# Performance work log

Hardware: AMD Instinct MI355X
Metric: run time of the kernel (lower is better)

## Reference

```python
import jax, jax.numpy as jnp
import numpy as np
from jax.ops import segment_sum

N = 50000        # nodes
E = 800000       # edges (avg degree 16)
H = 128          # hidden_dim
N_ITER = 2       # BCRefinement n_iterations
TIE_P = 0.05     # fraction of tie (boundary) edges


def setup_inputs() -> dict:
    key = jax.random.key(0)
    ks = jax.random.split(key, 24)
    s = 0.02
    inp = {
        'h': jax.random.normal(ks[0], (N, H), jnp.float32),
        'e': jax.random.normal(ks[1], (E, H), jnp.float32),
        'edge_attr_raw': jax.random.normal(ks[2], (E, 10), jnp.float32),
        # edge_refine: Linear(3H,2H) -> ReLU -> Linear(2H,H)
        'W_er1': s * jax.random.normal(ks[3], (3 * H, 2 * H), jnp.float32),
        'b_er1': jnp.zeros((2 * H,), jnp.float32),
        'W_er2': s * jax.random.normal(ks[4], (2 * H, H), jnp.float32),
        'b_er2': jnp.zeros((H,), jnp.float32),
        # GRUCell(H,H) torch layout: [3H, H] chunks (r, z, n)
        'W_ih': s * jax.random.normal(ks[5], (3 * H, H), jnp.float32),
        'W_hh': s * jax.random.normal(ks[6], (3 * H, H), jnp.float32),
        'b_ih': jnp.zeros((3 * H,), jnp.float32),
        'b_hh': jnp.zeros((3 * H,), jnp.float32),
        # node_neigh_fc: Linear(H,H)
        'W_nn': s * jax.random.normal(ks[7], (H, H), jnp.float32),
        'b_nn': jnp.zeros((H,), jnp.float32),
        # gate_mlp: Linear(3H,H) -> ReLU -> Linear(H,1), last bias init -2.0
        'W_g1': s * jax.random.normal(ks[8], (3 * H, H), jnp.float32),
        'b_g1': jnp.zeros((H,), jnp.float32),
        'W_g2': s * jax.random.normal(ks[9], (H, 1), jnp.float32),
        'b_g2': jnp.full((1,), -2.0, jnp.float32),
        'edge_index': jax.random.randint(ks[10], (2, E), 0, N, jnp.int32),
        'is_tie': jax.random.uniform(ks[11], (E,)) < TIE_P,
    }
    return inp


def reference(h, e, edge_attr_raw,
              W_er1, b_er1, W_er2, b_er2,
              W_ih, W_hh, b_ih, b_hh,
              W_nn, b_nn,
              W_g1, b_g1, W_g2, b_g2,
              edge_index, is_tie):
    row = edge_index[0]
    col = edge_index[1]
    tie_f = is_tie.astype(h.dtype)                        # [E]
    internal = ~is_tie

    # coupling buses: endpoints of any tie edge (tie-incidence count > 0)
    cpl_cnt = segment_sum(tie_f, row, num_segments=N) + \
              segment_sum(tie_f, col, num_segments=N)     # [N]
    is_cpl = cpl_cnt > 0

    # internal edges pointing into coupling buses; b_smooth weights w = 1/sqrt(X^2+eps)
    to_cpl = internal & is_cpl[col]
    X = jnp.abs(edge_attr_raw[:, 1])
    w = jnp.where(to_cpl, 1.0 / jnp.sqrt(X * X + 1e-6), 0.0)
    w_den = segment_sum(w, col, num_segments=N)           # [N]
    w_norm = w / (w_den[col] + 1e-6)                      # [E], zero off-mask

    deg = jnp.maximum(cpl_cnt, 1.0)                       # clamp_min(1.0)

    h_work, e_work = h, e
    for _ in range(N_ITER):
        # --- tie-edge refinement (applied only on tie edges) ---
        edge_in = jnp.concatenate([e_work, h_work[row], h_work[col]], axis=-1)  # [E,3H]
        e_ref = jax.nn.relu(edge_in @ W_er1 + b_er1) @ W_er2 + b_er2            # [E,H]
        e_work = e_work + tie_f[:, None] * e_ref

        # --- node messages from internal neighbors into coupling buses ---
        m_node_msg = h_work[row] @ W_nn + b_nn                                   # [E,H]
        m_node_all = segment_sum(m_node_msg * w_norm[:, None], col,
                                 num_segments=N)                                 # [N,H]

        # --- mean of incident tie-edge features at each node ---
        tie_e = tie_f[:, None] * e_work                                          # [E,H]
        m_edge_all = (segment_sum(tie_e, row, num_segments=N) +
                      segment_sum(tie_e, col, num_segments=N)) / deg[:, None]    # [N,H]

        # --- gating + GRU update on coupling buses ---
        gate_in = jnp.concatenate([m_edge_all, m_node_all, h_work], axis=-1)     # [N,3H]
        gate = jax.nn.sigmoid(jax.nn.relu(gate_in @ W_g1 + b_g1) @ W_g2 + b_g2)  # [N,1]
        m = m_edge_all + gate * m_node_all                                       # [N,H]

        gi = m @ W_ih.T + b_ih                                                   # [N,3H]
        gh = h_work @ W_hh.T + b_hh
        r = jax.nn.sigmoid(gi[:, :H] + gh[:, :H])
        z = jax.nn.sigmoid(gi[:, H:2 * H] + gh[:, H:2 * H])
        n = jnp.tanh(gi[:, 2 * H:] + r * gh[:, 2 * H:])
        h_new = (1.0 - z) * n + z * h_work

        h_work = jnp.where(is_cpl[:, None], h_new, h_work)
    return h_work, e_work
```

## Files before the change

kernel.cpp:

```cpp
#include <hip/hip_runtime.h>
#include <cstdint>

#define N_NODES 50000
#define N_EDGES 800000
#define HDIM    128
#define TIE_CAP 44000
#define NITER   2
#define SCAN_B  256

typedef __attribute__((ext_vector_type(8))) short bf16x8;
typedef __attribute__((ext_vector_type(4))) float f32x4;

__device__ __forceinline__ uint32_t f2bf(float f) {
    uint32_t u = __builtin_bit_cast(uint32_t, f);
    return (u + 0x7fffu + ((u >> 16) & 1u)) >> 16;
}
__device__ __forceinline__ float bf2f(uint32_t b) {
    return __builtin_bit_cast(float, b << 16);
}
__device__ __forceinline__ uint32_t comb2(uint32_t me, uint32_t mn, float g) {
    float a0 = bf2f(me & 0xffffu) + g * bf2f(mn & 0xffffu);
    float a1 = bf2f(me >> 16)     + g * bf2f(mn >> 16);
    return f2bf(a0) | (f2bf(a1) << 16);
}


__device__ __forceinline__ void stage_a128(const float* __restrict__ base,
                                           const int* __restrict__ gidx,
                                           int m0, int Mlim, char* tile, int tid)
{
    const int c = tid & 15;
    #pragma unroll
    for (int p = 0; p < 4; ++p) {
        int row = p * 32 + (tid >> 4);
        int ar = m0 + row; if (ar >= Mlim) ar = Mlim - 1;
        long g = gidx ? gidx[ar] : ar;
        const float* s = base + g * HDIM + c * 4;
        float4 v0 = *(const float4*)s;
        float4 v1 = *(const float4*)(s + 64);
        uint2 w0 = make_uint2(f2bf(v0.x) | (f2bf(v0.y) << 16),
                              f2bf(v0.z) | (f2bf(v0.w) << 16));
        uint2 w1 = make_uint2(f2bf(v1.x) | (f2bf(v1.y) << 16),
                              f2bf(v1.z) | (f2bf(v1.w) << 16));
        int sw = (row & 7) << 4;
        *(uint2*)(tile + row * 256 + ((c * 8) ^ sw)) = w0;
        *(uint2*)(tile + row * 256 + ((c * 8 + 128) ^ sw)) = w1;
    }
}

__device__ __forceinline__ void stage_bf128(const uint16_t* __restrict__ base,
                                            const int* __restrict__ gidx,
                                            int m0, int Mlim, char* tile, int tid)
{
    const int c = tid & 15;
    #pragma unroll
    for (int p = 0; p < 4; ++p) {
        int row = p * 32 + (tid >> 4);
        int ar = m0 + row; if (ar >= Mlim) ar = Mlim - 1;
        long g = gidx ? gidx[ar] : ar;
        uint4 v = *(const uint4*)(base + g * HDIM + c * 8);
        *(uint4*)(tile + row * 256 + ((c * 16) ^ ((row & 7) << 4))) = v;
    }
}

__device__ __forceinline__ void stage_b128(const short* __restrict__ BT, int ldk,
                                           int n0, int k0, char* tile, int tid)
{
    const int c = tid & 15;
    #pragma unroll
    for (int p = 0; p < 4; ++p) {
        int n = p * 32 + (tid >> 4);
        uint4 v = *(const uint4*)&BT[(size_t)(n0 + n) * ldk + k0 + c * 8];
        *(uint4*)(tile + n * 256 + ((c * 16) ^ ((n & 7) << 4))) = v;
    }
}

__device__ __forceinline__ void mfma128(const char* At, const char* Bt,
                                        int wr, int wc, int lane, f32x4 acc[4][2])
{
    #pragma unroll
    for (int ks = 0; ks < 4; ++ks) {
        int kb = ks * 64 + (lane >> 4) * 16;
        bf16x8 aF[4], bF[2];
        #pragma unroll
        for (int mi = 0; mi < 4; ++mi) {
            int row = wr * 64 + mi * 16 + (lane & 15);
            aF[mi] = *(const bf16x8*)(At + row * 256 + (kb ^ ((row & 7) << 4)));
        }
        #pragma unroll
        for (int ni = 0; ni < 2; ++ni) {
            int n = wc * 32 + ni * 16 + (lane & 15);
            bF[ni] = *(const bf16x8*)(Bt + n * 256 + (kb ^ ((n & 7) << 4)));
        }
        #pragma unroll
        for (int mi = 0; mi < 4; ++mi)
            #pragma unroll
            for (int ni = 0; ni < 2; ++ni)
                acc[mi][ni] = __builtin_amdgcn_mfma_f32_16x16x32_bf16(
                    aF[mi], bF[ni], acc[mi][ni], 0, 0, 0);
    }
}

__global__ __launch_bounds__(512)
void k_tie_fused(float* __restrict__ out_e, const uint16_t* __restrict__ h_bf,
                 const int* __restrict__ tie_cnt_p,
                 const int* __restrict__ tie_list, const int* __restrict__ tie_row,
                 const int* __restrict__ tie_col,
                 const short* __restrict__ BTer1, const short* __restrict__ BTer2,
                 const float* __restrict__ b_er1, const float* __restrict__ b_er2,
                 const float* __restrict__ deg_inv, float* __restrict__ m_edge)
{
    int cnt = *tie_cnt_p; if (cnt > TIE_CAP) cnt = TIE_CAP;
    const int m0 = blockIdx.x * 128;
    if (m0 >= cnt) return;

    __shared__ __align__(16) char At[32 * 1024];
    __shared__ __align__(16) char B0[32 * 1024];
    __shared__ __align__(16) char B1[32 * 1024];

    const int tid = threadIdx.x, lane = tid & 63;
    const int wid = tid >> 6, wr = wid >> 2, wc = wid & 3;

    f32x4 acc0[4][2] = {}, acc1[4][2] = {};
    #pragma unroll 1
    for (int c = 0; c < 3; ++c) {
        if (c == 0) stage_a128(out_e, tie_list, m0, cnt, At, tid);
        else        stage_bf128(h_bf, (c == 1) ? tie_row : tie_col, m0, cnt, At, tid);
        stage_b128(BTer1, 384, 0,   c * 128, B0, tid);
        stage_b128(BTer1, 384, 128, c * 128, B1, tid);
        __syncthreads();
        mfma128(At, B0, wr, wc, lane, acc0);
        mfma128(At, B1, wr, wc, lane, acc1);
        __syncthreads();
    }

    #pragma unroll
    for (int half = 0; half < 2; ++half) {
        char* Ct = half ? B0 : At;
        #pragma unroll
        for (int ni = 0; ni < 2; ++ni) {
            int col = wc * 32 + ni * 16 + (lane & 15);
            float bv = b_er1[half * 128 + col];
            #pragma unroll
            for (int mi = 0; mi < 4; ++mi)
                #pragma unroll
                for (int j = 0; j < 4; ++j) {
                    int rl = wr * 64 + mi * 16 + ((lane >> 4) << 2) + j;
                    float v = fmaxf((half ? acc1 : acc0)[mi][ni][j] + bv, 0.f);
                    *(uint16_t*)(Ct + rl * 256 + ((col * 2) ^ ((rl & 7) << 4))) =
                        (uint16_t)f2bf(v);
                }
        }
    }
    stage_b128(BTer2, 256, 0, 0, B1, tid);
    __syncthreads();
    f32x4 acc2[4][2] = {};
    mfma128(At, B1, wr, wc, lane, acc2);
    __syncthreads();
    stage_b128(BTer2, 256, 0, 128, B1, tid);
    __syncthreads();
    mfma128(B0, B1, wr, wc, lane, acc2);

    int col0 = wc * 32 + (lane & 15);
    float bv0 = b_er2[col0], bv1 = b_er2[col0 + 16];
    #pragma unroll
    for (int mi = 0; mi < 4; ++mi) {
        #pragma unroll
        for (int j = 0; j < 4; ++j) {
            int i = m0 + wr * 64 + mi * 16 + ((lane >> 4) << 2) + j;
            if (i < cnt) {
                int e = tie_list[i], r = tie_row[i], cc = tie_col[i];
                float dr = deg_inv[r], dc = deg_inv[cc];
                #pragma unroll
                for (int ni = 0; ni < 2; ++ni) {
                    int col = col0 + ni * 16;
                    float er = acc2[mi][ni][j] + (ni ? bv1 : bv0);
                    size_t eb = (size_t)e * HDIM + col;
                    float v = out_e[eb] + er;
                    out_e[eb] = v;
                    atomicAdd(&m_edge[(size_t)r * HDIM + col], v * dr);
                    atomicAdd(&m_edge[(size_t)cc * HDIM + col], v * dc);
                }
            }
        }
    }
}

__global__ __launch_bounds__(512)
void k_node_mega(float* __restrict__ m_edge, const uint16_t* __restrict__ agg,
                 float* __restrict__ out_h, uint16_t* __restrict__ h_bf,
                 const float* __restrict__ cpl_cnt, const float* __restrict__ sumw,
                 const short* __restrict__ BTnn, const float* __restrict__ b_nn,
                 const short* __restrict__ BTg1, const float* __restrict__ b_g1,
                 const float* __restrict__ Wg2, const float* __restrict__ b_g2,
                 const short* __restrict__ BTcomb,
                 const short* __restrict__ BTihn, const short* __restrict__ BThhn,
                 const float* __restrict__ b_ih, const float* __restrict__ b_hh)
{
    const int m0 = blockIdx.x * 128;
    __shared__ __align__(16) char Tme[32 * 1024];
    __shared__ __align__(16) char Tmn[32 * 1024];
    __shared__ __align__(16) char Th [32 * 1024];
    __shared__ __align__(16) char Bt [32 * 1024];
    __shared__ float g_red[4][128];
    __shared__ float g_fin[128];
    __shared__ float sw_s[128];

    const int tid = threadIdx.x, lane = tid & 63;
    const int wid = tid >> 6, wr = wid >> 2, wc = wid & 3;

    stage_a128(m_edge, nullptr, m0, N_NODES, Tme, tid);
    stage_bf128(agg,   nullptr, m0, N_NODES, Tmn, tid);
    stage_bf128(h_bf,  nullptr, m0, N_NODES, Th,  tid);
    stage_b128(BTnn, 128, 0, 0, Bt, tid);
    if (tid < 128) {
        int n = m0 + tid; if (n >= N_NODES) n = N_NODES - 1;
        sw_s[tid] = sumw[n];
    }
    __syncthreads();

    {
        int lim = (N_NODES - m0 < 128 ? N_NODES - m0 : 128) * HDIM / 4;
        float4* mp = (float4*)(m_edge + (size_t)m0 * HDIM);
        for (int i2 = tid; i2 < lim; i2 += 512)
            mp[i2] = make_float4(0.f, 0.f, 0.f, 0.f);
    }

    {
        f32x4 accM[4][2] = {};
        mfma128(Tmn, Bt, wr, wc, lane, accM);
        __syncthreads();
        #pragma unroll
        for (int ni = 0; ni < 2; ++ni) {
            int col = wc * 32 + ni * 16 + (lane & 15);
            float bv = b_nn[col];
            #pragma unroll
            for (int mi = 0; mi < 4; ++mi)
                #pragma unroll
                for (int j = 0; j < 4; ++j) {
                    int rl = wr * 64 + mi * 16 + ((lane >> 4) << 2) + j;
                    float v = accM[mi][ni][j] + sw_s[rl] * bv;
                    *(uint16_t*)(Tmn + rl * 256 + ((col * 2) ^ ((rl & 7) << 4))) =
                        (uint16_t)f2bf(v);
                }
        }
        __syncthreads();
    }

    f32x4 accG[4][2] = {};
    #pragma unroll 1
    for (int c = 0; c < 3; ++c) {
        const char* Ac = (c == 0) ? Tme : (c == 1) ? Tmn : Th;
        stage_b128(BTg1, 384, 0, c * 128, Bt, tid);
        __syncthreads();
        mfma128(Ac, Bt, wr, wc, lane, accG);
        __syncthreads();
    }
    {
        float bg[2], wg[2];
        #pragma unroll
        for (int ni = 0; ni < 2; ++ni) {
            int col = wc * 32 + ni * 16 + (lane & 15);
            bg[ni] = b_g1[col]; wg[ni] = Wg2[col];
        }
        #pragma unroll
        for (int mi = 0; mi < 4; ++mi)
            #pragma unroll
            for (int j = 0; j < 4; ++j) {
                float p = fmaxf(accG[mi][0][j] + bg[0], 0.f) * wg[0]
                        + fmaxf(accG[mi][1][j] + bg[1], 0.f) * wg[1];
                #pragma unroll
                for (int o = 8; o; o >>= 1) p += __shfl_xor(p, o);
                if ((lane & 15) == 0)
                    g_red[wc][wr * 64 + mi * 16 + ((lane >> 4) << 2) + j] = p;
            }
    }
    __syncthreads();
    if (tid < 128) {
        float t = g_red[0][tid] + g_red[1][tid] + g_red[2][tid] + g_red[3][tid]
                + b_g2[0];
        g_fin[tid] = 1.f / (1.f + __expf(-t));
    }
    __syncthreads();

    {
        const int c = tid & 15;
        #pragma unroll
        for (int p = 0; p < 4; ++p) {
            int row = p * 32 + (tid >> 4);
            float g = g_fin[row];
            int sw = (row & 7) << 4;
            #pragma unroll
            for (int hh = 0; hh < 2; ++hh) {
                int off = (c * 8 + hh * 128) ^ sw;
                uint2 me2 = *(uint2*)(Tme + row * 256 + off);
                uint2 mn2 = *(uint2*)(Tmn + row * 256 + off);
                *(uint2*)(Tmn + row * 256 + off) =
                    make_uint2(comb2(me2.x, mn2.x, g), comb2(me2.y, mn2.y, g));
            }
        }
    }
    __syncthreads();

    f32x4 aR[4][2] = {}, aZ[4][2] = {}, aGI[4][2] = {}, aGH[4][2] = {};
    stage_b128(BTcomb, 256, 0, 0, Bt, tid);   __syncthreads();
    mfma128(Tmn, Bt, wr, wc, lane, aR);       __syncthreads();
    stage_b128(BTcomb, 256, 0, 128, Bt, tid); __syncthreads();
    mfma128(Th, Bt, wr, wc, lane, aR);        __syncthreads();
    stage_b128(BTcomb, 256, 128, 0, Bt, tid); __syncthreads();
    mfma128(Tmn, Bt, wr, wc, lane, aZ);       __syncthreads();
    stage_b128(BTcomb, 256, 128, 128, Bt, tid); __syncthreads();
    mfma128(Th, Bt, wr, wc, lane, aZ);        __syncthreads();
    stage_b128(BTihn, 128, 0, 0, Bt, tid);    __syncthreads();
    mfma128(Tmn, Bt, wr, wc, lane, aGI);      __syncthreads();
    stage_b128(BThhn, 128, 0, 0, Bt, tid);    __syncthreads();
    mfma128(Th, Bt, wr, wc, lane, aGH);

    #pragma unroll
    for (int ni = 0; ni < 2; ++ni) {
        int col = wc * 32 + ni * 16 + (lane & 15);
        float br  = b_ih[col] + b_hh[col];
        float bz  = b_ih[128 + col] + b_hh[128 + col];
        float bin = b_ih[256 + col], bhn = b_hh[256 + col];
        #pragma unroll
        for (int mi = 0; mi < 4; ++mi)
            #pragma unroll
            for (int j = 0; j < 4; ++j) {
                int node = m0 + wr * 64 + mi * 16 + ((lane >> 4) << 2) + j;
                if (node < N_NODES && cpl_cnt[node] > 0.f) {
                    float r = 1.f / (1.f + __expf(-(aR[mi][ni][j] + br)));
                    float z = 1.f / (1.f + __expf(-(aZ[mi][ni][j] + bz)));
                    float nn = tanhf(aGI[mi][ni][j] + bin + r * (aGH[mi][ni][j] + bhn));
                    size_t hb = (size_t)node * HDIM + col;
                    float hv = out_h[hb];
                    float hn = (1.f - z) * nn + z * hv;
                    out_h[hb] = hn;
                    h_bf[hb] = (uint16_t)f2bf(hn);
                }
            }
    }
}

__global__ __launch_bounds__(256)
void k_mnode_gather(const int* __restrict__ row_ptr, const int* __restrict__ csr_row,
                    const float* __restrict__ csr_w, const uint16_t* __restrict__ h_bf,
                    uint16_t* __restrict__ agg)
{
    int n = blockIdx.x * 4 + (threadIdx.x >> 6);
    if (n >= N_NODES) return;
    int lane = threadIdx.x & 63;
    int s = row_ptr[n], t = row_ptr[n + 1];
    float a0 = 0.f, a1 = 0.f;
    for (int j = s; j < t; ++j) {
        int r = csr_row[j];
        float w = csr_w[j];
        uint32_t v = *(const uint32_t*)(h_bf + (size_t)r * HDIM + lane * 2);
        a0 += w * bf2f(v & 0xffffu);
        a1 += w * bf2f(v >> 16);
    }
    *(uint32_t*)(agg + (size_t)n * HDIM + lane * 2) = f2bf(a0) | (f2bf(a1) << 16);
}

#define INIT_BLOCKS 2753

__global__ __launch_bounds__(256)
void k_init(const float* __restrict__ e, float* __restrict__ out_e,
            const float* __restrict__ h, float* __restrict__ out_h,
            uint16_t* __restrict__ h_bf, float* __restrict__ m_edge,
            float* __restrict__ cpl_cnt, float* __restrict__ w_den,
            int* __restrict__ hist, int* __restrict__ counters,
            const uint8_t* __restrict__ tie_raw,
            const float* __restrict__ W_er1, const float* __restrict__ W_er2,
            const float* __restrict__ W_nn, const float* __restrict__ W_g1,
            const float* __restrict__ W_ih, const float* __restrict__ W_hh,
            short* __restrict__ BTer1, short* __restrict__ BTer2,
            short* __restrict__ BTnn, short* __restrict__ BTg1,
            short* __restrict__ BTcomb, short* __restrict__ BTihn,
            short* __restrict__ BThhn)
{
    const int b = blockIdx.x, t = threadIdx.x;
    if (b < 2048) {
        const float4* src = (const float4*)e;
        float4* dst = (float4*)out_e;
        for (int i = b * 256 + t; i < N_EDGES * HDIM / 4; i += 2048 * 256)
            dst[i] = src[i];
    } else if (b < 2304) {
        for (int i = (b - 2048) * 256 + t; i < N_NODES * HDIM / 4; i += 256 * 256) {
            float4 v = ((const float4*)h)[i];
            ((float4*)out_h)[i] = v;
            *(uint2*)(h_bf + (size_t)i * 4) =
                make_uint2(f2bf(v.x) | (f2bf(v.y) << 16),
                           f2bf(v.z) | (f2bf(v.w) << 16));
        }
    } else if (b < 2560) {
        for (int i = (b - 2304) * 256 + t; i < N_NODES * HDIM / 4; i += 256 * 256)
            ((float4*)m_edge)[i] = make_float4(0.f, 0.f, 0.f, 0.f);
    } else if (b < 2624) {
        for (int i = (b - 2560) * 256 + t; i < N_NODES; i += 64 * 256) {
            cpl_cnt[i] = 0.f; w_den[i] = 0.f; hist[i] = 0;
        }
    } else if (b < 2752) {
        for (int i = (b - 2624) * 256 + t; i < 384 * 256; i += 128 * 256) {
            {   int n = i / 384, k = i % 384;
                BTer1[i] = (short)f2bf(W_er1[(size_t)k * 256 + n]); }
            if (i < 128 * 256) {
                int n = i / 256, k = i % 256;
                BTer2[i] = (short)f2bf(W_er2[(size_t)k * 128 + n]); }
            if (i < 128 * 128) {
                int n = i / 128, k = i % 128;
                BTnn[i] = (short)f2bf(W_nn[(size_t)k * 128 + n]); }
            if (i < 128 * 384) {
                int n = i / 384, k = i % 384;
                BTg1[i] = (short)f2bf(W_g1[(size_t)k * 128 + n]); }
            if (i < 256 * 256) {
                int n = i >> 8, k = i & 255;
                float v = (k < 128) ? W_ih[n * 128 + k] : W_hh[n * 128 + (k - 128)];
                BTcomb[i] = (short)f2bf(v); }
            if (i < 128 * 128) {
                BTihn[i] = (short)f2bf(W_ih[256 * 128 + i]);
                BThhn[i] = (short)f2bf(W_hh[256 * 128 + i]); }
        }
    } else {
        if (t < 64) {
            int c = 0;
            for (int k = t; k < 4096; k += 64)
                if ((k & 3) && tie_raw[k]) c = 1;
            unsigned long long m = __ballot(c != 0);
            if (t == 0) {
                counters[0] = (m != 0ull) ? 1 : 0;
                counters[1] = 0; counters[2] = 0;
            }
        }
    }
}

__global__ __launch_bounds__(256)
void k_tie(const void* __restrict__ tie_raw, const int* __restrict__ counters,
           const int* __restrict__ ei, float* __restrict__ cpl_cnt,
           int* __restrict__ tie_cnt, int* __restrict__ tie_list,
           int* __restrict__ tie_row, int* __restrict__ tie_col)
{
    int e = blockIdx.x * 256 + threadIdx.x;
    int fmt = counters[0];
    bool t = false; int r = 0, c = 0;
    if (e < N_EDGES)
        t = fmt ? (((const uint8_t*)tie_raw)[e] != 0)
                : (((const int*)tie_raw)[e] != 0);
    if (t) {
        r = ei[e]; c = ei[N_EDGES + e];
        atomicAdd(&cpl_cnt[r], 1.f);
        atomicAdd(&cpl_cnt[c], 1.f);
    }
    unsigned long long m = __ballot(t);
    if (m == 0ull) return;
    int lane = threadIdx.x & 63;
    int first = __ffsll((unsigned long long)m) - 1;
    int base = 0;
    if (lane == first) base = atomicAdd(tie_cnt, __popcll(m));
    base = __shfl(base, first);
    if (t) {
        int idx = base + __popcll(m & ((1ull << lane) - 1ull));
        if (idx < TIE_CAP) { tie_list[idx] = e; tie_row[idx] = r; tie_col[idx] = c; }
    }
}

__global__ __launch_bounds__(256)
void k_w(const void* __restrict__ tie_raw, const int* __restrict__ counters,
         const int* __restrict__ ei, const float* __restrict__ attr,
         const float* __restrict__ cpl_cnt, float* __restrict__ w_den,
         float* __restrict__ w_arr, int* __restrict__ hist)
{
    int e = blockIdx.x * 256 + threadIdx.x;
    if (e >= N_EDGES) return;
    int fmt = counters[0];
    bool t = fmt ? (((const uint8_t*)tie_raw)[e] != 0)
                 : (((const int*)tie_raw)[e] != 0);
    float w = 0.f;
    if (!t) {
        int c = ei[N_EDGES + e];
        if (cpl_cnt[c] > 0.f) {
            float X = fabsf(attr[(size_t)e * 10 + 1]);
            w = 1.f / sqrtf(X * X + 1e-6f);
            atomicAdd(&w_den[c], w);
            atomicAdd(&hist[c], 1);
        }
    }
    w_arr[e] = w;
}

__global__ __launch_bounds__(SCAN_B)
void k_scan1(const int* __restrict__ hist, int* __restrict__ excl,
             int* __restrict__ bsum)
{
    __shared__ int s[SCAN_B];
    int t = threadIdx.x;
    int i = blockIdx.x * SCAN_B + t;
    int v = (i < N_NODES) ? hist[i] : 0;
    s[t] = v;
    __syncthreads();
    for (int o = 1; o < SCAN_B; o <<= 1) {
        int u = (t >= o) ? s[t - o] : 0;
        __syncthreads();
        s[t] += u;
        __syncthreads();
    }
    if (i < N_NODES) excl[i] = s[t] - v;
    if (t == SCAN_B - 1) bsum[blockIdx.x] = s[t];
}

__global__ void k_scan2(int* __restrict__ bsum, int* __restrict__ counters)
{
    const int NB = (N_NODES + SCAN_B - 1) / SCAN_B;
    if (threadIdx.x == 0) {
        int run = 0;
        for (int b = 0; b < NB; ++b) { int x = bsum[b]; bsum[b] = run; run += x; }
        counters[2] = run;
    }
}

__global__ __launch_bounds__(256)
void k_scan3(const int* __restrict__ excl, const int* __restrict__ bsum,
             int* __restrict__ row_ptr, int* __restrict__ cursor,
             const int* __restrict__ counters,
             const float* __restrict__ cpl_cnt, const float* __restrict__ w_den,
             float* __restrict__ deg_inv, float* __restrict__ sumw)
{
    int i = blockIdx.x * 256 + threadIdx.x;
    if (i < N_NODES) {
        int v = excl[i] + bsum[i >> 8];
        row_ptr[i] = v;
        cursor[i] = v;
        deg_inv[i] = 1.f / fmaxf(cpl_cnt[i], 1.f);
        float wd = w_den[i];
        sumw[i] = wd / (wd + 1e-6f);
    }
    if (i == N_NODES) row_ptr[N_NODES] = counters[2];
}

__global__ __launch_bounds__(256)
void k_fill(const int* __restrict__ ei, const float* __restrict__ w_arr,
            const float* __restrict__ w_den, int* __restrict__ cursor,
            int* __restrict__ csr_row, float* __restrict__ csr_w)
{
    int e = blockIdx.x * 256 + threadIdx.x;
    if (e >= N_EDGES) return;
    float w = w_arr[e];
    if (w == 0.f) return;
    int c = ei[N_EDGES + e];
    int pos = atomicAdd(&cursor[c], 1);
    csr_row[pos] = ei[e];
    csr_w[pos] = w / (w_den[c] + 1e-6f);
}

extern "C" void kernel_launch(void* const* d_in, const int* in_sizes, int n_in,
                              void* d_out, int out_size, void* d_ws, size_t ws_size,
                              hipStream_t stream)
{
    const float* h     = (const float*)d_in[0];
    const float* e     = (const float*)d_in[1];
    const float* attr  = (const float*)d_in[2];
    const float* W_er1 = (const float*)d_in[3];
    const float* b_er1 = (const float*)d_in[4];
    const float* W_er2 = (const float*)d_in[5];
    const float* b_er2 = (const float*)d_in[6];
    const float* W_ih  = (const float*)d_in[7];
    const float* W_hh  = (const float*)d_in[8];
    const float* b_ih  = (const float*)d_in[9];
    const float* b_hh  = (const float*)d_in[10];
    const float* W_nn  = (const float*)d_in[11];
    const float* b_nn  = (const float*)d_in[12];
    const float* W_g1  = (const float*)d_in[13];
    const float* b_g1  = (const float*)d_in[14];
    const float* W_g2  = (const float*)d_in[15];
    const float* b_g2  = (const float*)d_in[16];
    const int*   ei    = (const int*)d_in[17];
    const void*  tie_raw = d_in[18];

    float* out_h = (float*)d_out;
    float* out_e = out_h + (size_t)N_NODES * HDIM;

    char* ws = (char*)d_ws;
    size_t off = 0;
    auto alloc = [&](size_t bytes) -> void* {
        void* p = ws + off;
        off = (off + bytes + 255) & ~(size_t)255;
        return p;
    };
    float* cpl_cnt = (float*)alloc((size_t)N_NODES * 4);
    float* w_den   = (float*)alloc((size_t)N_NODES * 4);
    int*   hist    = (int*)  alloc((size_t)N_NODES * 4);
    int*   counters= (int*)  alloc(256);
    float* deg_inv = (float*)alloc((size_t)N_NODES * 4);
    float* sumw    = (float*)alloc((size_t)N_NODES * 4);
    float* w_arr   = (float*)alloc((size_t)N_EDGES * 4);
    int* tie_list  = (int*)alloc((size_t)TIE_CAP * 4);
    int* tie_row   = (int*)alloc((size_t)TIE_CAP * 4);
    int* tie_col   = (int*)alloc((size_t)TIE_CAP * 4);
    short* BTer1   = (short*)alloc((size_t)256 * 384 * 2);
    short* BTer2   = (short*)alloc((size_t)128 * 256 * 2);
    short* BTnn    = (short*)alloc((size_t)128 * 128 * 2);
    short* BTg1    = (short*)alloc((size_t)128 * 384 * 2);
    short* BTcomb  = (short*)alloc((size_t)256 * 256 * 2);
    short* BTihn   = (short*)alloc((size_t)128 * 128 * 2);
    short* BThhn   = (short*)alloc((size_t)128 * 128 * 2);
    uint16_t* h_bf = (uint16_t*)alloc((size_t)N_NODES * HDIM * 2);
    uint16_t* agg  = (uint16_t*)alloc((size_t)N_NODES * HDIM * 2);
    float* m_edge  = (float*)alloc((size_t)N_NODES * HDIM * 4);
    int* excl      = (int*)alloc((size_t)N_NODES * 4);
    int* bsum      = (int*)alloc(256 * 4);
    int* row_ptr   = (int*)alloc((size_t)(N_NODES + 1) * 4);
    int* cursor    = (int*)alloc((size_t)N_NODES * 4);
    int* csr_row   = (int*)alloc((size_t)N_EDGES * 4);
    float* csr_w   = (float*)alloc((size_t)N_EDGES * 4);
    if (off > ws_size) return;

    int* tie_cnt = counters + 1;

    const int EB   = N_EDGES / 256;
    const int GM_T = (TIE_CAP + 127) / 128;
    const int GM_N = (N_NODES + 127) / 128;
    const int NB   = (N_NODES + SCAN_B - 1) / SCAN_B;

    k_init<<<INIT_BLOCKS, 256, 0, stream>>>(
        e, out_e, h, out_h, h_bf, m_edge, cpl_cnt, w_den, hist, counters,
        (const uint8_t*)tie_raw,
        W_er1, W_er2, W_nn, W_g1, W_ih, W_hh,
        BTer1, BTer2, BTnn, BTg1, BTcomb, BTihn, BThhn);
    k_tie<<<EB, 256, 0, stream>>>(tie_raw, counters, ei, cpl_cnt,
                                  tie_cnt, tie_list, tie_row, tie_col);
    k_w<<<EB, 256, 0, stream>>>(tie_raw, counters, ei, attr, cpl_cnt,
                                w_den, w_arr, hist);
    k_scan1<<<NB, SCAN_B, 0, stream>>>(hist, excl, bsum);
    k_scan2<<<1, 64, 0, stream>>>(bsum, counters);
    k_scan3<<<(N_NODES + 256) / 256, 256, 0, stream>>>(
        excl, bsum, row_ptr, cursor, counters, cpl_cnt, w_den, deg_inv, sumw);
    k_fill<<<EB, 256, 0, stream>>>(ei, w_arr, w_den, cursor, csr_row, csr_w);

    for (int it = 0; it < NITER; ++it) {
        k_tie_fused<<<GM_T, 512, 0, stream>>>(
            out_e, h_bf, tie_cnt, tie_list, tie_row, tie_col,
            BTer1, BTer2, b_er1, b_er2, deg_inv, m_edge);
        k_mnode_gather<<<(N_NODES + 3) / 4, 256, 0, stream>>>(
            row_ptr, csr_row, csr_w, h_bf, agg);
        k_node_mega<<<GM_N, 512, 0, stream>>>(
            m_edge, agg, out_h, h_bf, cpl_cnt, sumw,
            BTnn, b_nn, BTg1, b_g1, W_g2, b_g2,
            BTcomb, BTihn, BThhn, b_ih, b_hh);
    }
}
```

Baseline: 911.6 us.

## Replace tie-edge atomic scatter with CSR gather and double-buffer GRU weight staging

Builds a second CSR indexing tie edges by incident node during setup. The per-node mean of tie-edge features is now gathered inside the m_node gather kernel instead of being scatter-added with float atomics in the tie GEMM epilogue. That removes the fp32 m_edge buffer, its zeroing passes and the atomics, and stores the mean in bf16. The node kernel also alternates two shared buffers for weight staging so fewer barriers are needed between MFMA phases. The costs are an extra scan and fill pass and a bf16 rounding of the edge mean.

```diff
diff --git a/kernel.cpp b/kernel.cpp
--- a/kernel.cpp
+++ b/kernel.cpp
@@ -7,6 +7,8 @@
 #define TIE_CAP 44000
 #define NITER   2
 #define SCAN_B  256
+#define EB_CONST 3125
+#define TB_CONST 172
 
 typedef __attribute__((ext_vector_type(8))) short bf16x8;
 typedef __attribute__((ext_vector_type(4))) float f32x4;
@@ -107,8 +109,7 @@
                  const int* __restrict__ tie_list, const int* __restrict__ tie_row,
                  const int* __restrict__ tie_col,
                  const short* __restrict__ BTer1, const short* __restrict__ BTer2,
-                 const float* __restrict__ b_er1, const float* __restrict__ b_er2,
-                 const float* __restrict__ deg_inv, float* __restrict__ m_edge)
+                 const float* __restrict__ b_er1, const float* __restrict__ b_er2)
 {
     int cnt = *tie_cnt_p; if (cnt > TIE_CAP) cnt = TIE_CAP;
     const int m0 = blockIdx.x * 128;
@@ -169,25 +170,56 @@
         for (int j = 0; j < 4; ++j) {
             int i = m0 + wr * 64 + mi * 16 + ((lane >> 4) << 2) + j;
             if (i < cnt) {
-                int e = tie_list[i], r = tie_row[i], cc = tie_col[i];
-                float dr = deg_inv[r], dc = deg_inv[cc];
+                int e = tie_list[i];
                 #pragma unroll
                 for (int ni = 0; ni < 2; ++ni) {
                     int col = col0 + ni * 16;
-                    float er = acc2[mi][ni][j] + (ni ? bv1 : bv0);
                     size_t eb = (size_t)e * HDIM + col;
-                    float v = out_e[eb] + er;
-                    out_e[eb] = v;
-                    atomicAdd(&m_edge[(size_t)r * HDIM + col], v * dr);
-                    atomicAdd(&m_edge[(size_t)cc * HDIM + col], v * dc);
+                    out_e[eb] += acc2[mi][ni][j] + (ni ? bv1 : bv0);
                 }
             }
         }
     }
 }
 
+__global__ __launch_bounds__(256)
+void k_gather(const int* __restrict__ row_ptr, const int* __restrict__ csr_row,
+              const float* __restrict__ csr_w, const uint16_t* __restrict__ h_bf,
+              uint16_t* __restrict__ agg,
+              const int* __restrict__ row_ptr2, const int* __restrict__ tcsr,
+              const float* __restrict__ out_e, const float* __restrict__ deg_inv,
+              uint16_t* __restrict__ m_edge_bf)
+{
+    int n = blockIdx.x * 4 + (threadIdx.x >> 6);
+    if (n >= N_NODES) return;
+    int lane = threadIdx.x & 63;
+
+    int s = row_ptr[n], t = row_ptr[n + 1];
+    float a0 = 0.f, a1 = 0.f;
+    for (int j = s; j < t; ++j) {
+        int r = csr_row[j];
+        float w = csr_w[j];
+        uint32_t v = *(const uint32_t*)(h_bf + (size_t)r * HDIM + lane * 2);
+        a0 += w * bf2f(v & 0xffffu);
+        a1 += w * bf2f(v >> 16);
+    }
+    *(uint32_t*)(agg + (size_t)n * HDIM + lane * 2) = f2bf(a0) | (f2bf(a1) << 16);
+
+    int s2 = row_ptr2[n], t2 = row_ptr2[n + 1];
+    float b0 = 0.f, b1 = 0.f;
+    for (int j = s2; j < t2; ++j) {
+        int e = tcsr[j];
+        float2 v = *(const float2*)(out_e + (size_t)e * HDIM + lane * 2);
+        b0 += v.x; b1 += v.y;
+    }
+    float di = deg_inv[n];
+    *(uint32_t*)(m_edge_bf + (size_t)n * HDIM + lane * 2) =
+        f2bf(b0 * di) | (f2bf(b1 * di) << 16);
+}
+
 __global__ __launch_bounds__(512)
-void k_node_mega(float* __restrict__ m_edge, const uint16_t* __restrict__ agg,
+void k_node_mega(const uint16_t* __restrict__ m_edge_bf,
+                 const uint16_t* __restrict__ agg,
                  float* __restrict__ out_h, uint16_t* __restrict__ h_bf,
                  const float* __restrict__ cpl_cnt, const float* __restrict__ sumw,
                  const short* __restrict__ BTnn, const float* __restrict__ b_nn,
@@ -209,22 +241,15 @@
     const int tid = threadIdx.x, lane = tid & 63;
     const int wid = tid >> 6, wr = wid >> 2, wc = wid & 3;
 
-    stage_a128(m_edge, nullptr, m0, N_NODES, Tme, tid);
-    stage_bf128(agg,   nullptr, m0, N_NODES, Tmn, tid);
-    stage_bf128(h_bf,  nullptr, m0, N_NODES, Th,  tid);
+    stage_bf128(m_edge_bf, nullptr, m0, N_NODES, Tme, tid);
+    stage_bf128(agg,       nullptr, m0, N_NODES, Tmn, tid);
+    stage_bf128(h_bf,      nullptr, m0, N_NODES, Th,  tid);
     stage_b128(BTnn, 128, 0, 0, Bt, tid);
     if (tid < 128) {
         int n = m0 + tid; if (n >= N_NODES) n = N_NODES - 1;
         sw_s[tid] = sumw[n];
     }
     __syncthreads();
-
-    {
-        int lim = (N_NODES - m0 < 128 ? N_NODES - m0 : 128) * HDIM / 4;
-        float4* mp = (float4*)(m_edge + (size_t)m0 * HDIM);
-        for (int i2 = tid; i2 < lim; i2 += 512)
-            mp[i2] = make_float4(0.f, 0.f, 0.f, 0.f);
-    }
 
     {
         f32x4 accM[4][2] = {};
@@ -283,6 +308,7 @@
     }
     __syncthreads();
 
+    stage_b128(BTcomb, 256, 0, 0, Bt, tid);
     {
         const int c = tid & 15;
         #pragma unroll
@@ -303,18 +329,17 @@
     __syncthreads();
 
     f32x4 aR[4][2] = {}, aZ[4][2] = {}, aGI[4][2] = {}, aGH[4][2] = {};
-    stage_b128(BTcomb, 256, 0, 0, Bt, tid);   __syncthreads();
-    mfma128(Tmn, Bt, wr, wc, lane, aR);       __syncthreads();
-    stage_b128(BTcomb, 256, 0, 128, Bt, tid); __syncthreads();
-    mfma128(Th, Bt, wr, wc, lane, aR);        __syncthreads();
-    stage_b128(BTcomb, 256, 128, 0, Bt, tid); __syncthreads();
-    mfma128(Tmn, Bt, wr, wc, lane, aZ);       __syncthreads();
-    stage_b128(BTcomb, 256, 128, 128, Bt, tid); __syncthreads();
-    mfma128(Th, Bt, wr, wc, lane, aZ);        __syncthreads();
-    stage_b128(BTihn, 128, 0, 0, Bt, tid);    __syncthreads();
-    mfma128(Tmn, Bt, wr, wc, lane, aGI);      __syncthreads();
-    stage_b128(BThhn, 128, 0, 0, Bt, tid);    __syncthreads();
-    mfma128(Th, Bt, wr, wc, lane, aGH);
+    stage_b128(BTcomb, 256, 0, 128, Tme, tid);
+    mfma128(Tmn, Bt, wr, wc, lane, aR);   __syncthreads();
+    stage_b128(BTcomb, 256, 128, 0, Bt, tid);
+    mfma128(Th, Tme, wr, wc, lane, aR);   __syncthreads();
+    stage_b128(BTcomb, 256, 128, 128, Tme, tid);
+    mfma128(Tmn, Bt, wr, wc, lane, aZ);   __syncthreads();
+    stage_b128(BTihn, 128, 0, 0, Bt, tid);
+    mfma128(Th, Tme, wr, wc, lane, aZ);   __syncthreads();
+    stage_b128(BThhn, 128, 0, 0, Tme, tid);
+    mfma128(Tmn, Bt, wr, wc, lane, aGI);  __syncthreads();
+    mfma128(Th, Tme, wr, wc, lane, aGH);
 
     #pragma unroll
     for (int ni = 0; ni < 2; ++ni) {
@@ -341,32 +366,12 @@
     }
 }
 
-__global__ __launch_bounds__(256)
-void k_mnode_gather(const int* __restrict__ row_ptr, const int* __restrict__ csr_row,
-                    const float* __restrict__ csr_w, const uint16_t* __restrict__ h_bf,
-                    uint16_t* __restrict__ agg)
-{
-    int n = blockIdx.x * 4 + (threadIdx.x >> 6);
-    if (n >= N_NODES) return;
-    int lane = threadIdx.x & 63;
-    int s = row_ptr[n], t = row_ptr[n + 1];
-    float a0 = 0.f, a1 = 0.f;
-    for (int j = s; j < t; ++j) {
-        int r = csr_row[j];
-        float w = csr_w[j];
-        uint32_t v = *(const uint32_t*)(h_bf + (size_t)r * HDIM + lane * 2);
-        a0 += w * bf2f(v & 0xffffu);
-        a1 += w * bf2f(v >> 16);
-    }
-    *(uint32_t*)(agg + (size_t)n * HDIM + lane * 2) = f2bf(a0) | (f2bf(a1) << 16);
-}
-
-#define INIT_BLOCKS 2753
+#define INIT_BLOCKS 2497
 
 __global__ __launch_bounds__(256)
 void k_init(const float* __restrict__ e, float* __restrict__ out_e,
             const float* __restrict__ h, float* __restrict__ out_h,
-            uint16_t* __restrict__ h_bf, float* __restrict__ m_edge,
+            uint16_t* __restrict__ h_bf,
             float* __restrict__ cpl_cnt, float* __restrict__ w_den,
             int* __restrict__ hist, int* __restrict__ counters,
             const uint8_t* __restrict__ tie_raw,
@@ -392,15 +397,12 @@
                 make_uint2(f2bf(v.x) | (f2bf(v.y) << 16),
                            f2bf(v.z) | (f2bf(v.w) << 16));
         }
-    } else if (b < 2560) {
-        for (int i = (b - 2304) * 256 + t; i < N_NODES * HDIM / 4; i += 256 * 256)
-            ((float4*)m_edge)[i] = make_float4(0.f, 0.f, 0.f, 0.f);
-    } else if (b < 2624) {
-        for (int i = (b - 2560) * 256 + t; i < N_NODES; i += 64 * 256) {
+    } else if (b < 2368) {
+        for (int i = (b - 2304) * 256 + t; i < N_NODES; i += 64 * 256) {
             cpl_cnt[i] = 0.f; w_den[i] = 0.f; hist[i] = 0;
         }
-    } else if (b < 2752) {
-        for (int i = (b - 2624) * 256 + t; i < 384 * 256; i += 128 * 256) {
+    } else if (b < 2496) {
+        for (int i = (b - 2368) * 256 + t; i < 384 * 256; i += 128 * 256) {
             {   int n = i / 384, k = i % 384;
                 BTer1[i] = (short)f2bf(W_er1[(size_t)k * 256 + n]); }
             if (i < 128 * 256) {
@@ -428,7 +430,7 @@
             unsigned long long m = __ballot(c != 0);
             if (t == 0) {
                 counters[0] = (m != 0ull) ? 1 : 0;
-                counters[1] = 0; counters[2] = 0;
+                counters[1] = 0; counters[2] = 0; counters[3] = 0;
             }
         }
     }
@@ -489,8 +491,9 @@
 }
 
 __global__ __launch_bounds__(SCAN_B)
-void k_scan1(const int* __restrict__ hist, int* __restrict__ excl,
-             int* __restrict__ bsum)
+void k_scan1(const int* __restrict__ hist, const float* __restrict__ cpl_cnt,
+             int* __restrict__ excl, int* __restrict__ bsum,
+             int* __restrict__ excl2, int* __restrict__ bsum2)
 {
     __shared__ int s[SCAN_B];
     int t = threadIdx.x;
@@ -506,21 +509,39 @@
     }
     if (i < N_NODES) excl[i] = s[t] - v;
     if (t == SCAN_B - 1) bsum[blockIdx.x] = s[t];
-}
-
-__global__ void k_scan2(int* __restrict__ bsum, int* __restrict__ counters)
+    __syncthreads();
+    int v2 = (i < N_NODES) ? (int)cpl_cnt[i] : 0;
+    s[t] = v2;
+    __syncthreads();
+    for (int o = 1; o < SCAN_B; o <<= 1) {
+        int u = (t >= o) ? s[t - o] : 0;
+        __syncthreads();
+        s[t] += u;
+        __syncthreads();
+    }
+    if (i < N_NODES) excl2[i] = s[t] - v2;
+    if (t == SCAN_B - 1) bsum2[blockIdx.x] = s[t];
+}
+
+__global__ void k_scan2(int* __restrict__ bsum, int* __restrict__ bsum2,
+                        int* __restrict__ counters)
 {
     const int NB = (N_NODES + SCAN_B - 1) / SCAN_B;
     if (threadIdx.x == 0) {
         int run = 0;
         for (int b = 0; b < NB; ++b) { int x = bsum[b]; bsum[b] = run; run += x; }
         counters[2] = run;
+        int run2 = 0;
+        for (int b = 0; b < NB; ++b) { int x = bsum2[b]; bsum2[b] = run2; run2 += x; }
+        counters[3] = run2;
     }
 }
 
 __global__ __launch_bounds__(256)
 void k_scan3(const int* __restrict__ excl, const int* __restrict__ bsum,
+             const int* __restrict__ excl2, const int* __restrict__ bsum2,
              int* __restrict__ row_ptr, int* __restrict__ cursor,
+             int* __restrict__ row_ptr2, int* __restrict__ cursor2,
              const int* __restrict__ counters,
              const float* __restrict__ cpl_cnt, const float* __restrict__ w_den,
              float* __restrict__ deg_inv, float* __restrict__ sumw)
@@ -528,28 +549,46 @@
     int i = blockIdx.x * 256 + threadIdx.x;
     if (i < N_NODES) {
         int v = excl[i] + bsum[i >> 8];
-        row_ptr[i] = v;
-        cursor[i] = v;
+        row_ptr[i] = v;  cursor[i] = v;
+        int v2 = excl2[i] + bsum2[i >> 8];
+        row_ptr2[i] = v2; cursor2[i] = v2;
         deg_inv[i] = 1.f / fmaxf(cpl_cnt[i], 1.f);
         float wd = w_den[i];
         sumw[i] = wd / (wd + 1e-6f);
     }
-    if (i == N_NODES) row_ptr[N_NODES] = counters[2];
+    if (i == N_NODES) {
+        row_ptr[N_NODES] = counters[2];
+        row_ptr2[N_NODES] = counters[3];
+    }
 }
 
 __global__ __launch_bounds__(256)
 void k_fill(const int* __restrict__ ei, const float* __restrict__ w_arr,
             const float* __restrict__ w_den, int* __restrict__ cursor,
-            int* __restrict__ csr_row, float* __restrict__ csr_w)
-{
-    int e = blockIdx.x * 256 + threadIdx.x;
-    if (e >= N_EDGES) return;
-    float w = w_arr[e];
-    if (w == 0.f) return;
-    int c = ei[N_EDGES + e];
-    int pos = atomicAdd(&cursor[c], 1);
-    csr_row[pos] = ei[e];
-    csr_w[pos] = w / (w_den[c] + 1e-6f);
+            int* __restrict__ csr_row, float* __restrict__ csr_w,
+            const int* __restrict__ counters, const int* __restrict__ tie_list,
+            const int* __restrict__ tie_row, const int* __restrict__ tie_col,
+            int* __restrict__ cursor2, int* __restrict__ tcsr)
+{
+    int b = blockIdx.x;
+    if (b < EB_CONST) {
+        int e = b * 256 + threadIdx.x;
+        if (e >= N_EDGES) return;
+        float w = w_arr[e];
+        if (w == 0.f) return;
+        int c = ei[N_EDGES + e];
+        int pos = atomicAdd(&cursor[c], 1);
+        csr_row[pos] = ei[e];
+        csr_w[pos] = w / (w_den[c] + 1e-6f);
+    } else {
+        int i = (b - EB_CONST) * 256 + threadIdx.x;
+        int cnt = counters[1]; if (cnt > TIE_CAP) cnt = TIE_CAP;
+        if (i < cnt) {
+            int e = tie_list[i];
+            int p1 = atomicAdd(&cursor2[tie_row[i]], 1); tcsr[p1] = e;
+            int p2 = atomicAdd(&cursor2[tie_col[i]], 1); tcsr[p2] = e;
+        }
+    }
 }
 
 extern "C" void kernel_launch(void* const* d_in, const int* in_sizes, int n_in,
@@ -605,45 +644,53 @@
     short* BThhn   = (short*)alloc((size_t)128 * 128 * 2);
     uint16_t* h_bf = (uint16_t*)alloc((size_t)N_NODES * HDIM * 2);
     uint16_t* agg  = (uint16_t*)alloc((size_t)N_NODES * HDIM * 2);
-    float* m_edge  = (float*)alloc((size_t)N_NODES * HDIM * 4);
+    uint16_t* m_edge_bf = (uint16_t*)alloc((size_t)N_NODES * HDIM * 2);
     int* excl      = (int*)alloc((size_t)N_NODES * 4);
+    int* excl2     = (int*)alloc((size_t)N_NODES * 4);
     int* bsum      = (int*)alloc(256 * 4);
+    int* bsum2     = (int*)alloc(256 * 4);
     int* row_ptr   = (int*)alloc((size_t)(N_NODES + 1) * 4);
+    int* row_ptr2  = (int*)alloc((size_t)(N_NODES + 1) * 4);
     int* cursor    = (int*)alloc((size_t)N_NODES * 4);
+    int* cursor2   = (int*)alloc((size_t)N_NODES * 4);
     int* csr_row   = (int*)alloc((size_t)N_EDGES * 4);
     float* csr_w   = (float*)alloc((size_t)N_EDGES * 4);
+    int* tcsr      = (int*)alloc((size_t)2 * TIE_CAP * 4);
     if (off > ws_size) return;
 
     int* tie_cnt = counters + 1;
 
-    const int EB   = N_EDGES / 256;
     const int GM_T = (TIE_CAP + 127) / 128;
     const int GM_N = (N_NODES + 127) / 128;
     const int NB   = (N_NODES + SCAN_B - 1) / SCAN_B;
 
     k_init<<<INIT_BLOCKS, 256, 0, stream>>>(
-        e, out_e, h, out_h, h_bf, m_edge, cpl_cnt, w_den, hist, counters,
+        e, out_e, h, out_h, h_bf, cpl_cnt, w_den, hist, counters,
         (const uint8_t*)tie_raw,
         W_er1, W_er2, W_nn, W_g1, W_ih, W_hh,
         BTer1, BTer2, BTnn, BTg1, BTcomb, BTihn, BThhn);
-    k_tie<<<EB, 256, 0, stream>>>(tie_raw, counters, ei, cpl_cnt,
-                                  tie_cnt, tie_list, tie_row, tie_col);
-    k_w<<<EB, 256, 0, stream>>>(tie_raw, counters, ei, attr, cpl_cnt,
-                                w_den, w_arr, hist);
-    k_scan1<<<NB, SCAN_B, 0, stream>>>(hist, excl, bsum);
-    k_scan2<<<1, 64, 0, stream>>>(bsum, counters);
+    k_tie<<<EB_CONST, 256, 0, stream>>>(tie_raw, counters, ei, cpl_cnt,
+                                        tie_cnt, tie_list, tie_row, tie_col);
+    k_w<<<EB_CONST, 256, 0, stream>>>(tie_raw, counters, ei, attr, cpl_cnt,
+                                      w_den, w_arr, hist);
+    k_scan1<<<NB, SCAN_B, 0, stream>>>(hist, cpl_cnt, excl, bsum, excl2, bsum2);
+    k_scan2<<<1, 64, 0, stream>>>(bsum, bsum2, counters);
     k_scan3<<<(N_NODES + 256) / 256, 256, 0, stream>>>(
-        excl, bsum, row_ptr, cursor, counters, cpl_cnt, w_den, deg_inv, sumw);
-    k_fill<<<EB, 256, 0, stream>>>(ei, w_arr, w_den, cursor, csr_row, csr_w);
+        excl, bsum, excl2, bsum2, row_ptr, cursor, row_ptr2, cursor2,
+        counters, cpl_cnt, w_den, deg_inv, sumw);
+    k_fill<<<EB_CONST + TB_CONST, 256, 0, stream>>>(
+        ei, w_arr, w_den, cursor, csr_row, csr_w,
+        counters, tie_list, tie_row, tie_col, cursor2, tcsr);
 
     for (int it = 0; it < NITER; ++it) {
         k_tie_fused<<<GM_T, 512, 0, stream>>>(
             out_e, h_bf, tie_cnt, tie_list, tie_row, tie_col,
-            BTer1, BTer2, b_er1, b_er2, deg_inv, m_edge);
-        k_mnode_gather<<<(N_NODES + 3) / 4, 256, 0, stream>>>(
-            row_ptr, csr_row, csr_w, h_bf, agg);
+            BTer1, BTer2, b_er1, b_er2);
+        k_gather<<<(N_NODES + 3) / 4, 256, 0, stream>>>(
+            row_ptr, csr_row, csr_w, h_bf, agg,
+            row_ptr2, tcsr, out_e, deg_inv, m_edge_bf);
         k_node_mega<<<GM_N, 512, 0, stream>>>(
-            m_edge, agg, out_h, h_bf, cpl_cnt, sumw,
+            m_edge_bf, agg, out_h, h_bf, cpl_cnt, sumw,
             BTnn, b_nn, BTg1, b_g1, W_g2, b_g2,
             BTcomb, BTihn, BThhn, b_ih, b_hh);
     }
```

Measured after the change: 843.8 us. 7.4% less time.
